# Kernel optimization log

Measured on AMD Instinct MI355X. Metric: run time of the kernel, lower is better.

Reference implementation:

```python
import jax, jax.numpy as jnp
import numpy as np

D = 128
P = 1.0
EPS_PD = 1e-6   # torch pairwise_distance eps
EPS_NORM = 1e-12  # torch F.normalize eps


def setup_inputs() -> dict:
    key = jax.random.key(0)
    k1, k2, k3, k4 = jax.random.split(key, 4)
    B = 8192
    triplet_idx = jax.random.randint(k1, (B, 5), 0, 1000, dtype=jnp.int64)
    entity_emb = jax.random.normal(k2, (500000, D), dtype=jnp.float32)
    relation_emb = jax.random.normal(k3, (1000, D), dtype=jnp.float32)
    time_transfer = jax.random.normal(k4, (1000, D * D), dtype=jnp.float32)
    return {"triplet_idx": triplet_idx, "entity_emb": entity_emb,
            "relation_emb": relation_emb, "time_transfer": time_transfer}


def _l2norm(x):
    n = jnp.sqrt(jnp.sum(x * x, axis=-1, keepdims=True))
    return x / jnp.maximum(n, EPS_NORM)


def reference(triplet_idx, entity_emb, relation_emb, time_transfer):
    h = entity_emb[triplet_idx[:, 0]]          # [B, D]
    r = relation_emb[triplet_idx[:, 1]]        # [B, D]
    t = entity_emb[triplet_idx[:, 2]]          # [B, D]
    B = h.shape[0]
    Ts = time_transfer[triplet_idx[:, 3]].reshape(B, D, D)
    Te = time_transfer[triplet_idx[:, 4]].reshape(B, D, D)
    M = Ts + Te                                # [B, D, D]
    h2 = _l2norm(jnp.einsum('bd,bde->be', h, M))
    t2 = _l2norm(jnp.einsum('bd,bde->be', t, M))
    diff = h2 + r - t2 + EPS_PD
    # torch pairwise_distance: (sum |diff|^p)^(1/p); p=1 -> sum abs
    score = jnp.sum(jnp.abs(diff) ** P, axis=-1) ** (1.0 / P)
    return score
```

## Files before the change

kernel.cpp:

```cpp
#include <hip/hip_runtime.h>

#define D 128
#define CAP_R 128

__global__ __launch_bounds__(256) void transe_time_kernel(
    const int* __restrict__ idx, const float* __restrict__ ent,
    const float* __restrict__ rel, const float* __restrict__ tt,
    float* __restrict__ out, int B)
{
    const int b = blockIdx.x;
    if (b >= B) return;
    const int tid = threadIdx.x;
    const int e4  = tid & 31;
    const int g   = tid >> 5;

    __shared__ float sh_h[D];
    __shared__ float sh_t[D];
    __shared__ float ph[8][D];
    __shared__ float pt[8][D];
    __shared__ float wred[8];

    const int hi = idx[b * 5 + 0];
    const int ri = idx[b * 5 + 1];
    const int ti = idx[b * 5 + 2];
    const int si = idx[b * 5 + 3];
    const int ei = idx[b * 5 + 4];

    if (tid < D) {
        sh_h[tid] = ent[(size_t)hi * D + tid];
        sh_t[tid] = ent[(size_t)ti * D + tid];
    }
    __syncthreads();

    const float4* __restrict__ Ts = (const float4*)(tt + (size_t)si * D * D);
    const float4* __restrict__ Te = (const float4*)(tt + (size_t)ei * D * D);

    float4 hacc = make_float4(0.f, 0.f, 0.f, 0.f);
    float4 tacc = make_float4(0.f, 0.f, 0.f, 0.f);

    #pragma unroll 4
    for (int d0 = 0; d0 < D; d0 += 8) {
        const int d = d0 + g;
        const float4 a = Ts[d * 32 + e4];
        const float4 c = Te[d * 32 + e4];
        const float hd = sh_h[d];
        const float td = sh_t[d];
        const float mx = a.x + c.x;
        const float my = a.y + c.y;
        const float mz = a.z + c.z;
        const float mw = a.w + c.w;
        hacc.x += hd * mx; hacc.y += hd * my; hacc.z += hd * mz; hacc.w += hd * mw;
        tacc.x += td * mx; tacc.y += td * my; tacc.z += td * mz; tacc.w += td * mw;
    }

    ((float4*)ph[g])[e4] = hacc;
    ((float4*)pt[g])[e4] = tacc;
    __syncthreads();

    float h2 = 0.f, t2 = 0.f;
    if (tid < D) {
        #pragma unroll
        for (int k = 0; k < 8; ++k) { h2 += ph[k][tid]; t2 += pt[k][tid]; }
    }
    float nh = h2 * h2;
    float nt = t2 * t2;
    #pragma unroll
    for (int off = 32; off; off >>= 1) {
        nh += __shfl_down(nh, off, 64);
        nt += __shfl_down(nt, off, 64);
    }
    const int wv = tid >> 6;
    if ((tid & 63) == 0) { wred[wv * 2] = nh; wred[wv * 2 + 1] = nt; }
    __syncthreads();
    const float NH = wred[0] + wred[2] + wred[4] + wred[6];
    const float NT2 = wred[1] + wred[3] + wred[5] + wred[7];
    const float rnh = 1.0f / fmaxf(sqrtf(NH), 1e-12f);
    const float rnt = 1.0f / fmaxf(sqrtf(NT2), 1e-12f);

    float v = 0.f;
    if (tid < D) {
        const float rr = rel[(size_t)ri * D + tid];
        v = fabsf(h2 * rnh + rr - t2 * rnt + 1e-6f);
    }
    #pragma unroll
    for (int off = 32; off; off >>= 1) v += __shfl_down(v, off, 64);
    __syncthreads();
    if ((tid & 63) == 0) wred[wv] = v;
    __syncthreads();
    if (tid == 0) out[b] = wred[0] + wred[1] + wred[2] + wred[3];
}


__global__ __launch_bounds__(1024) void zero_cnt_kernel(int* __restrict__ cnt, int NT)
{
    const int t = threadIdx.x;
    if (t < NT) cnt[t] = 0;
}

__global__ __launch_bounds__(256) void scatter_kernel(
    const int* __restrict__ idx, int* __restrict__ cnt,
    int2* __restrict__ rowsbuf, int B)
{
    const int i = blockIdx.x * blockDim.x + threadIdx.x;
    const int stride = gridDim.x * blockDim.x;
    for (int b = i; b < B; b += stride) {
        const int h_eid = idx[b * 5 + 0];
        const int t_eid = idx[b * 5 + 2];
        #pragma unroll
        for (int slot = 0; slot < 2; ++slot) {
            const int u = idx[b * 5 + 3 + slot];
            const int p = atomicAdd(&cnt[u], 2);
            if (p + 1 < CAP_R) {
                rowsbuf[u * CAP_R + p]     = make_int2(h_eid, (b * 2 + 0) * 2 + slot);
                rowsbuf[u * CAP_R + p + 1] = make_int2(t_eid, (b * 2 + 1) * 2 + slot);
            }
        }
    }
}

__device__ __forceinline__ void fma4(float4& a, float s, const float4& v) {
    a.x += s * v.x; a.y += s * v.y; a.z += s * v.z; a.w += s * v.w;
}

__global__ __launch_bounds__(256) void matvec_kernel(
    const float* __restrict__ ent, const float* __restrict__ tt,
    const int* __restrict__ cnt, const int2* __restrict__ rowsbuf,
    float* __restrict__ P)
{
    const int u = blockIdx.x;
    int n_rows = cnt[u];
    if (n_rows == 0) return;
    if (n_rows > CAP_R) n_rows = CAP_R;
    const int base = u * CAP_R;
    const int tid = threadIdx.x;

    const int w    = tid >> 6;
    const int lane = tid & 63;
    const int c8   = lane & 7;
    const int rh   = lane >> 3;
    const int col0 = w * 32 + c8 * 4;

    __shared__ float Esh[64][D + 4];
    __shared__ int   Dsh[64];
    const float* __restrict__ T = tt + (size_t)u * (D * D);

    for (int rr0 = 0; rr0 < n_rows; rr0 += 64) {
        {
            const int r  = tid >> 2;
            const int q  = tid & 3;
            const int rr = rr0 + r;
            if (rr < n_rows) {
                const int2 rec = rowsbuf[base + rr];
                const float* src = ent + (size_t)rec.x * D + q * 32;
                float4 v0 = *(const float4*)(src);
                float4 v1 = *(const float4*)(src + 4);
                float4 v2 = *(const float4*)(src + 8);
                float4 v3 = *(const float4*)(src + 12);
                float4 v4 = *(const float4*)(src + 16);
                float4 v5 = *(const float4*)(src + 20);
                float4 v6 = *(const float4*)(src + 24);
                float4 v7 = *(const float4*)(src + 28);
                float* drow = &Esh[r][q * 32];
                *(float4*)(drow)      = v0;
                *(float4*)(drow + 4)  = v1;
                *(float4*)(drow + 8)  = v2;
                *(float4*)(drow + 12) = v3;
                *(float4*)(drow + 16) = v4;
                *(float4*)(drow + 20) = v5;
                *(float4*)(drow + 24) = v6;
                *(float4*)(drow + 28) = v7;
                if (q == 0) Dsh[r] = rec.y;
            }
        }
        __syncthreads();

        float4 acc0 = make_float4(0.f, 0.f, 0.f, 0.f);
        float4 acc1 = acc0, acc2 = acc0, acc3 = acc0;
        float4 acc4 = acc0, acc5 = acc0, acc6 = acc0, acc7 = acc0;

        const float* Tc = T + col0;
        #pragma unroll 2
        for (int d4 = 0; d4 < D; d4 += 4) {
            const float* tp = Tc + (size_t)d4 * D;
            const float4 t0 = *(const float4*)(tp);
            const float4 t1 = *(const float4*)(tp + D);
            const float4 t2 = *(const float4*)(tp + 2 * D);
            const float4 t3 = *(const float4*)(tp + 3 * D);
            float4 e;
            e = *(const float4*)&Esh[rh][d4];
            fma4(acc0, e.x, t0); fma4(acc0, e.y, t1); fma4(acc0, e.z, t2); fma4(acc0, e.w, t3);
            e = *(const float4*)&Esh[rh + 8][d4];
            fma4(acc1, e.x, t0); fma4(acc1, e.y, t1); fma4(acc1, e.z, t2); fma4(acc1, e.w, t3);
            e = *(const float4*)&Esh[rh + 16][d4];
            fma4(acc2, e.x, t0); fma4(acc2, e.y, t1); fma4(acc2, e.z, t2); fma4(acc2, e.w, t3);
            e = *(const float4*)&Esh[rh + 24][d4];
            fma4(acc3, e.x, t0); fma4(acc3, e.y, t1); fma4(acc3, e.z, t2); fma4(acc3, e.w, t3);
            e = *(const float4*)&Esh[rh + 32][d4];
            fma4(acc4, e.x, t0); fma4(acc4, e.y, t1); fma4(acc4, e.z, t2); fma4(acc4, e.w, t3);
            e = *(const float4*)&Esh[rh + 40][d4];
            fma4(acc5, e.x, t0); fma4(acc5, e.y, t1); fma4(acc5, e.z, t2); fma4(acc5, e.w, t3);
            e = *(const float4*)&Esh[rh + 48][d4];
            fma4(acc6, e.x, t0); fma4(acc6, e.y, t1); fma4(acc6, e.z, t2); fma4(acc6, e.w, t3);
            e = *(const float4*)&Esh[rh + 56][d4];
            fma4(acc7, e.x, t0); fma4(acc7, e.y, t1); fma4(acc7, e.z, t2); fma4(acc7, e.w, t3);
        }

        #pragma unroll
        for (int k = 0; k < 8; ++k) {
            const float4& a = (k == 0) ? acc0 : (k == 1) ? acc1 : (k == 2) ? acc2 :
                              (k == 3) ? acc3 : (k == 4) ? acc4 : (k == 5) ? acc5 :
                              (k == 6) ? acc6 : acc7;
            const int r  = rh + 8 * k;
            const int rr = rr0 + r;
            if (rr < n_rows) {
                float* dst = P + (size_t)Dsh[r] * D + col0;
                *(float4*)dst = a;
            }
        }
        __syncthreads();
    }
}

__global__ __launch_bounds__(256) void score_kernel(
    const int* __restrict__ idx, const float* __restrict__ rel,
    const float* __restrict__ P, float* __restrict__ out, int B)
{
    const int tid = threadIdx.x;
    const int b = blockIdx.x * 4 + (tid >> 6);
    const int l = tid & 63;
    if (b >= B) return;

    const int ri = idx[b * 5 + 1];
    const float* ph = P + (size_t)(b * 2 + 0) * 2 * D;
    const float* pt = P + (size_t)(b * 2 + 1) * 2 * D;

    const float h0 = ph[l]      + ph[D + l];
    const float h1 = ph[64 + l] + ph[D + 64 + l];
    const float t0 = pt[l]      + pt[D + l];
    const float t1 = pt[64 + l] + pt[D + 64 + l];

    float nh = h0 * h0 + h1 * h1;
    float nt = t0 * t0 + t1 * t1;
    #pragma unroll
    for (int off = 32; off; off >>= 1) {
        nh += __shfl_down(nh, off, 64);
        nt += __shfl_down(nt, off, 64);
    }
    nh = __shfl(nh, 0, 64);
    nt = __shfl(nt, 0, 64);
    const float rnh = 1.0f / fmaxf(sqrtf(nh), 1e-12f);
    const float rnt = 1.0f / fmaxf(sqrtf(nt), 1e-12f);
    const float r0 = rel[(size_t)ri * D + l];
    const float r1 = rel[(size_t)ri * D + 64 + l];
    float v = fabsf(h0 * rnh + r0 - t0 * rnt + 1e-6f)
            + fabsf(h1 * rnh + r1 - t1 * rnt + 1e-6f);
    #pragma unroll
    for (int off = 32; off; off >>= 1) v += __shfl_down(v, off, 64);
    if (l == 0) out[b] = v;
}

extern "C" void kernel_launch(void* const* d_in, const int* in_sizes, int n_in,
                              void* d_out, int out_size, void* d_ws, size_t ws_size,
                              hipStream_t stream) {
    const int*   idx = (const int*)d_in[0];
    const float* ent = (const float*)d_in[1];
    const float* rel = (const float*)d_in[2];
    const float* tt  = (const float*)d_in[3];
    float* out = (float*)d_out;
    const int B  = in_sizes[0] / 5;
    const int NT = in_sizes[3] / (D * D);

    const size_t CNT_OFF  = 0;
    const size_t ROWS_OFF = 8192;
    const size_t ROWS_BYTES = (size_t)NT * CAP_R * sizeof(int2);
    const size_t P_OFF  = (ROWS_OFF + ROWS_BYTES + 255) & ~(size_t)255;
    const size_t need   = P_OFF + (size_t)B * 2 * 2 * D * sizeof(float);

    if (ws_size < need || NT > 1024) {
        transe_time_kernel<<<dim3(B), dim3(256), 0, stream>>>(idx, ent, rel, tt, out, B);
        return;
    }

    char* ws = (char*)d_ws;
    int*  cnt     = (int*)(ws + CNT_OFF);
    int2* rowsbuf = (int2*)(ws + ROWS_OFF);
    float* P      = (float*)(ws + P_OFF);

    zero_cnt_kernel<<<dim3(1),           dim3(1024), 0, stream>>>(cnt, NT);
    scatter_kernel <<<dim3(32),          dim3(256),  0, stream>>>(idx, cnt, rowsbuf, B);
    matvec_kernel  <<<dim3(NT),          dim3(256),  0, stream>>>(ent, tt, cnt, rowsbuf, P);
    score_kernel   <<<dim3((B + 3) / 4), dim3(256),  0, stream>>>(idx, rel, P, out, B);
}
```

Measured before the change: 53.40 us.

## Split matvec rows across two blocks per time matrix and specialize row-group count

The matvec grid gains a second dimension, so each time-transfer matrix is handled by two blocks that take interleaved 32-row chunks. This doubles parallelism and shrinks shared memory per block. A templated compute routine dispatches on the number of active 8-row groups, so blocks holding partial chunks skip FMAs on empty rows. The cost is that each matrix T is now read from global memory by two blocks instead of one, which adds L2 traffic.

Result: faster. 51.49 us (-3.6%).

```diff
diff --git a/kernel.cpp b/kernel.cpp
--- a/kernel.cpp
+++ b/kernel.cpp
@@ -122,6 +122,41 @@
     a.x += s * v.x; a.y += s * v.y; a.z += s * v.z; a.w += s * v.w;
 }
 
+template<int NG>
+__device__ __forceinline__ void compute_store(
+    const float* __restrict__ Tc, const float (*__restrict__ Esh)[D + 4],
+    const int* __restrict__ Dsh, float* __restrict__ P,
+    const int col0, const int rh, const int my_rows)
+{
+    float4 acc[NG];
+    #pragma unroll
+    for (int k = 0; k < NG; ++k) acc[k] = make_float4(0.f, 0.f, 0.f, 0.f);
+
+    #pragma unroll 2
+    for (int d4 = 0; d4 < D; d4 += 4) {
+        const float* tp = Tc + (size_t)d4 * D;
+        const float4 t0 = *(const float4*)(tp);
+        const float4 t1 = *(const float4*)(tp + D);
+        const float4 t2 = *(const float4*)(tp + 2 * D);
+        const float4 t3 = *(const float4*)(tp + 3 * D);
+        #pragma unroll
+        for (int k = 0; k < NG; ++k) {
+            const float4 e = *(const float4*)&Esh[rh + 8 * k][d4];
+            fma4(acc[k], e.x, t0); fma4(acc[k], e.y, t1);
+            fma4(acc[k], e.z, t2); fma4(acc[k], e.w, t3);
+        }
+    }
+
+    #pragma unroll
+    for (int k = 0; k < NG; ++k) {
+        const int r = rh + 8 * k;
+        if (r < my_rows) {
+            float* dst = P + (size_t)Dsh[r] * D + col0;
+            *(float4*)dst = acc[k];
+        }
+    }
+}
+
 __global__ __launch_bounds__(256) void matvec_kernel(
     const float* __restrict__ ent, const float* __restrict__ tt,
     const int* __restrict__ cnt, const int2* __restrict__ rowsbuf,
@@ -129,7 +164,6 @@
 {
     const int u = blockIdx.x;
     int n_rows = cnt[u];
-    if (n_rows == 0) return;
     if (n_rows > CAP_R) n_rows = CAP_R;
     const int base = u * CAP_R;
     const int tid = threadIdx.x;
@@ -140,82 +174,40 @@
     const int rh   = lane >> 3;
     const int col0 = w * 32 + c8 * 4;
 
-    __shared__ float Esh[64][D + 4];
-    __shared__ int   Dsh[64];
+    __shared__ float Esh[32][D + 4];
+    __shared__ int   Dsh[32];
     const float* __restrict__ T = tt + (size_t)u * (D * D);
-
-    for (int rr0 = 0; rr0 < n_rows; rr0 += 64) {
+    const float* __restrict__ Tc = T + col0;
+
+    for (int rr0 = blockIdx.y * 32; rr0 < n_rows; rr0 += 64) {
+        const int my_rows = min(32, n_rows - rr0);
+
         {
-            const int r  = tid >> 2;
-            const int q  = tid & 3;
-            const int rr = rr0 + r;
-            if (rr < n_rows) {
-                const int2 rec = rowsbuf[base + rr];
-                const float* src = ent + (size_t)rec.x * D + q * 32;
-                float4 v0 = *(const float4*)(src);
-                float4 v1 = *(const float4*)(src + 4);
-                float4 v2 = *(const float4*)(src + 8);
-                float4 v3 = *(const float4*)(src + 12);
-                float4 v4 = *(const float4*)(src + 16);
-                float4 v5 = *(const float4*)(src + 20);
-                float4 v6 = *(const float4*)(src + 24);
-                float4 v7 = *(const float4*)(src + 28);
-                float* drow = &Esh[r][q * 32];
+            const int r  = tid >> 3;
+            const int j8 = tid & 7;
+            if (r < my_rows) {
+                const int2 rec = rowsbuf[base + rr0 + r];
+                const float* src = ent + (size_t)rec.x * D + j8 * 16;
+                const float4 v0 = *(const float4*)(src);
+                const float4 v1 = *(const float4*)(src + 4);
+                const float4 v2 = *(const float4*)(src + 8);
+                const float4 v3 = *(const float4*)(src + 12);
+                float* drow = &Esh[r][j8 * 16];
                 *(float4*)(drow)      = v0;
                 *(float4*)(drow + 4)  = v1;
                 *(float4*)(drow + 8)  = v2;
                 *(float4*)(drow + 12) = v3;
-                *(float4*)(drow + 16) = v4;
-                *(float4*)(drow + 20) = v5;
-                *(float4*)(drow + 24) = v6;
-                *(float4*)(drow + 28) = v7;
-                if (q == 0) Dsh[r] = rec.y;
+                if (j8 == 0) Dsh[r] = rec.y;
             }
         }
         __syncthreads();
 
-        float4 acc0 = make_float4(0.f, 0.f, 0.f, 0.f);
-        float4 acc1 = acc0, acc2 = acc0, acc3 = acc0;
-        float4 acc4 = acc0, acc5 = acc0, acc6 = acc0, acc7 = acc0;
-
-        const float* Tc = T + col0;
-        #pragma unroll 2
-        for (int d4 = 0; d4 < D; d4 += 4) {
-            const float* tp = Tc + (size_t)d4 * D;
-            const float4 t0 = *(const float4*)(tp);
-            const float4 t1 = *(const float4*)(tp + D);
-            const float4 t2 = *(const float4*)(tp + 2 * D);
-            const float4 t3 = *(const float4*)(tp + 3 * D);
-            float4 e;
-            e = *(const float4*)&Esh[rh][d4];
-            fma4(acc0, e.x, t0); fma4(acc0, e.y, t1); fma4(acc0, e.z, t2); fma4(acc0, e.w, t3);
-            e = *(const float4*)&Esh[rh + 8][d4];
-            fma4(acc1, e.x, t0); fma4(acc1, e.y, t1); fma4(acc1, e.z, t2); fma4(acc1, e.w, t3);
-            e = *(const float4*)&Esh[rh + 16][d4];
-            fma4(acc2, e.x, t0); fma4(acc2, e.y, t1); fma4(acc2, e.z, t2); fma4(acc2, e.w, t3);
-            e = *(const float4*)&Esh[rh + 24][d4];
-            fma4(acc3, e.x, t0); fma4(acc3, e.y, t1); fma4(acc3, e.z, t2); fma4(acc3, e.w, t3);
-            e = *(const float4*)&Esh[rh + 32][d4];
-            fma4(acc4, e.x, t0); fma4(acc4, e.y, t1); fma4(acc4, e.z, t2); fma4(acc4, e.w, t3);
-            e = *(const float4*)&Esh[rh + 40][d4];
-            fma4(acc5, e.x, t0); fma4(acc5, e.y, t1); fma4(acc5, e.z, t2); fma4(acc5, e.w, t3);
-            e = *(const float4*)&Esh[rh + 48][d4];
-            fma4(acc6, e.x, t0); fma4(acc6, e.y, t1); fma4(acc6, e.z, t2); fma4(acc6, e.w, t3);
-            e = *(const float4*)&Esh[rh + 56][d4];
-            fma4(acc7, e.x, t0); fma4(acc7, e.y, t1); fma4(acc7, e.z, t2); fma4(acc7, e.w, t3);
-        }
-
-        #pragma unroll
-        for (int k = 0; k < 8; ++k) {
-            const float4& a = (k == 0) ? acc0 : (k == 1) ? acc1 : (k == 2) ? acc2 :
-                              (k == 3) ? acc3 : (k == 4) ? acc4 : (k == 5) ? acc5 :
-                              (k == 6) ? acc6 : acc7;
-            const int r  = rh + 8 * k;
-            const int rr = rr0 + r;
-            if (rr < n_rows) {
-                float* dst = P + (size_t)Dsh[r] * D + col0;
-                *(float4*)dst = a;
-            }
+        const int ng = (my_rows + 7) >> 3;
+        switch (ng) {
+            case 1: compute_store<1>(Tc, Esh, Dsh, P, col0, rh, my_rows); break;
+            case 2: compute_store<2>(Tc, Esh, Dsh, P, col0, rh, my_rows); break;
+            case 3: compute_store<3>(Tc, Esh, Dsh, P, col0, rh, my_rows); break;
+            default: compute_store<4>(Tc, Esh, Dsh, P, col0, rh, my_rows); break;
         }
         __syncthreads();
     }
@@ -288,6 +280,6 @@
 
     zero_cnt_kernel<<<dim3(1),           dim3(1024), 0, stream>>>(cnt, NT);
     scatter_kernel <<<dim3(32),          dim3(256),  0, stream>>>(idx, cnt, rowsbuf, B);
-    matvec_kernel  <<<dim3(NT),          dim3(256),  0, stream>>>(ent, tt, cnt, rowsbuf, P);
+    matvec_kernel  <<<dim3(NT, 2),       dim3(256),  0, stream>>>(ent, tt, cnt, rowsbuf, P);
     score_kernel   <<<dim3((B + 3) / 4), dim3(256),  0, stream>>>(idx, rel, P, out, B);
 }
```
